# Performance work log

Measured on AMD Instinct MI355X. Metric: run time of the kernel, lower is better.

Reference implementation:

```python
import jax, jax.numpy as jnp
import numpy as np

B, C, H, W = 4, 128, 128, 128
K = 9          # 3x3 kernel taps
TAU, BETA = 0.5, 10.0


def conv3x3(x, w, b):
    # x: (B,Cin,H,W), w: (Cout,Cin,3,3), stride 1, padding 1
    y = jax.lax.conv_general_dilated(
        x, w, window_strides=(1, 1), padding=((1, 1), (1, 1)),
        dimension_numbers=('NCHW', 'OIHW', 'NCHW'))
    return y + b[None, :, None, None]


def bilinear_sample(x, py, px):
    # x: (B,C,H,W); py,px: (B,K,H,W) fractional coords -> (B,C,K,H,W), zero outside
    Hi, Wi = x.shape[2], x.shape[3]
    y0 = jnp.floor(py); x0 = jnp.floor(px)
    y1 = y0 + 1.0;      x1 = x0 + 1.0
    ly = py - y0; lx = px - x0
    hy = 1.0 - ly; hx = 1.0 - lx
    xf = x.reshape(x.shape[0], x.shape[1], -1)  # (B,C,HW)

    def corner(yc, xc, wgt):
        valid = (yc >= 0) & (yc <= Hi - 1) & (xc >= 0) & (xc <= Wi - 1)
        yi = jnp.clip(yc, 0, Hi - 1).astype(jnp.int32)
        xi = jnp.clip(xc, 0, Wi - 1).astype(jnp.int32)
        idx = (yi * Wi + xi).reshape(yc.shape[0], -1)  # (B, K*H*W)
        g = jax.vmap(lambda f, i: f[:, i])(xf, idx)    # (B,C,K*H*W)
        g = g.reshape(x.shape[0], x.shape[1], *yc.shape[1:])  # (B,C,K,H,W)
        return g * (wgt * valid.astype(wgt.dtype))[:, None]

    return (corner(y0, x0, hy * hx) + corner(y0, x1, hy * lx)
            + corner(y1, x0, ly * hx) + corner(y1, x1, ly * lx))


def modulated_dcn(x, offset, mask, w, b):
    # offset: (B,2K,H,W) layout (dy,dx) per tap; mask: (B,K,H,W)
    Bn, Cn, Hn, Wn = x.shape
    off = offset.reshape(Bn, K, 2, Hn, Wn)
    dy, dx = off[:, :, 0], off[:, :, 1]
    ky, kx = jnp.meshgrid(jnp.arange(3), jnp.arange(3), indexing='ij')
    base_y = (ky.reshape(-1) - 1).astype(x.dtype)  # dilation=1, padding=1, stride=1
    base_x = (kx.reshape(-1) - 1).astype(x.dtype)
    hh = jnp.arange(Hn, dtype=x.dtype)
    ww = jnp.arange(Wn, dtype=x.dtype)
    py = hh[None, None, :, None] + base_y[None, :, None, None] + dy  # (B,K,H,W)
    px = ww[None, None, None, :] + base_x[None, :, None, None] + dx
    samp = bilinear_sample(x, py, px) * mask[:, None]  # (B,C,K,H,W)
    out = jnp.einsum('bckhw,ock->bohw', samp, w.reshape(w.shape[0], w.shape[1], K))
    return out + b[None, :, None, None]


def setup_inputs() -> dict:
    key = jax.random.key(0)
    ks = jax.random.split(key, 8)
    x = jax.random.normal(ks[0], (B, C, H, W), dtype=jnp.float32)
    U = jax.random.uniform(ks[1], (B, 1, H, W), dtype=jnp.float32)
    # conv_offset_mask: (3*K, C+1, 3, 3); small scale -> offsets of O(1) pixel
    w_om = jax.random.normal(ks[2], (3 * K, C + 1, 3, 3), dtype=jnp.float32) * 0.01
    b_om = jnp.zeros((3 * K,), dtype=jnp.float32)
    kaiming = float(np.sqrt(2.0 / (C * 9)))
    w_dcn = jax.random.normal(ks[3], (C, C, 3, 3), dtype=jnp.float32) * kaiming
    b_dcn = jnp.zeros((C,), dtype=jnp.float32)
    w1 = jax.random.normal(ks[4], (C, C, 3, 3), dtype=jnp.float32) * kaiming
    b1 = jnp.zeros((C,), dtype=jnp.float32)
    w2 = jax.random.normal(ks[5], (C, C, 3, 3), dtype=jnp.float32) * float(np.sqrt(1.0 / (C * 9)))
    b2 = jnp.zeros((C,), dtype=jnp.float32)
    return {"x": x, "U": U, "w_om": w_om, "b_om": b_om, "w_dcn": w_dcn,
            "b_dcn": b_dcn, "w1": w1, "b1": b1, "w2": w2, "b2": b2}


def reference(x, U, w_om, b_om, w_dcn, b_dcn, w1, b1, w2, b2):
    U = jnp.clip(U, 0.0, 1.0)
    guide = jnp.concatenate([x, U], axis=1)                # (B,C+1,H,W)
    om = conv3x3(guide, w_om, b_om)                        # (B,3K,H,W)
    offset = om[:, :2 * K]
    mask = 2.0 * jax.nn.sigmoid(om[:, 2 * K:])
    z = modulated_dcn(x, offset, mask, w_dcn, b_dcn)
    r = jax.nn.relu(conv3x3(z, w1, b1))
    r = conv3x3(r, w2, b2)
    gate = jax.nn.sigmoid(BETA * (U - TAU))
    return jax.nn.relu(x + r * gate)
```

## Files before the change

### kernel.cpp

```cpp
#include <hip/hip_runtime.h>
#include <math.h>

typedef unsigned int uint;
typedef unsigned short ushort;
typedef __attribute__((ext_vector_type(8))) __bf16 bf16x8;
typedef __attribute__((ext_vector_type(2))) __bf16 bf16x2;
typedef __attribute__((ext_vector_type(4))) float f32x4;
typedef __attribute__((ext_vector_type(2))) float f32x2;

#define HW 16384

__device__ __forceinline__ ushort f2bf(float f) {
    uint u = __float_as_uint(f);
    u += 0x7fffu + ((u >> 16) & 1u);
    return (ushort)(u >> 16);
}
__device__ __forceinline__ void bhmap(int& b, int& h) {
    int lin = blockIdx.y * (int)gridDim.x + blockIdx.x;
    int n = (lin & 7) * 64 + (lin >> 3);
    h = n & 127;
    b = n >> 7;
}
__device__ __forceinline__ int swz(int row, int chunk) {
    return row * 128 + ((chunk ^ (row & 15)) << 3);
}
__device__ __forceinline__ void gl2lds16(const ushort* g, ushort* l) {
    __builtin_amdgcn_global_load_lds(
        (const __attribute__((address_space(1))) uint*)g,
        (__attribute__((address_space(3))) uint*)l,
        16, 0, 0);
}
__device__ __forceinline__ uint blend2(uint a, uint b, uint c, uint d,
                                       float w00, float w01, float w10, float w11) {
    f32x2 va = { __uint_as_float(a << 16), __uint_as_float(a & 0xffff0000u) };
    f32x2 vb = { __uint_as_float(b << 16), __uint_as_float(b & 0xffff0000u) };
    f32x2 vc = { __uint_as_float(c << 16), __uint_as_float(c & 0xffff0000u) };
    f32x2 vd = { __uint_as_float(d << 16), __uint_as_float(d & 0xffff0000u) };
    f32x2 v = va * w00 + vb * w01 + vc * w10 + vd * w11;
    bf16x2 pk; pk[0] = (__bf16)v[0]; pk[1] = (__bf16)v[1];
    uint r; __builtin_memcpy(&r, &pk, 4);
    return r;
}

__global__ __launch_bounds__(256) void prep_w(
    const float* __restrict__ wd, const float* __restrict__ w1,
    const float* __restrict__ w2, const float* __restrict__ wom,
    ushort* __restrict__ wdt, ushort* __restrict__ w1t,
    ushort* __restrict__ w2t, ushort* __restrict__ womt,
    float* __restrict__ womu)
{
    int i = blockIdx.x * 256 + threadIdx.x;
    if (i < 147456) {
        int k = i >> 14, oc = (i >> 7) & 127, d = i & 127;
        int ci = (((d >> 3) ^ (oc & 15)) << 3) | (d & 7);
        int s = (oc * 128 + ci) * 9 + k;
        wdt[i] = f2bf(wd[s]);
        w1t[i] = f2bf(w1[s]);
        w2t[i] = f2bf(w2[s]);
    }
    if (i < 36864) {
        int k = i >> 12, oc = (i >> 7) & 31, d = i & 127;
        int ci = (((d >> 3) ^ (oc & 15)) << 3) | (d & 7);
        womt[i] = (oc < 27) ? f2bf(wom[(oc * 129 + ci) * 9 + k]) : (ushort)0;
    }
    if (i < 288) {
        int k = i >> 5, oc = i & 31;
        womu[i] = (oc < 27) ? wom[(oc * 129 + 128) * 9 + k] : 0.f;
    }
}

__global__ __launch_bounds__(256) void prep_xt(
    const float* __restrict__ x, ushort* __restrict__ xt)
{
    int b, h; bhmap(b, h);
    const int tid = threadIdx.x;
    __shared__ __align__(16) ushort T[128 * 136];
    const int w0 = tid & 127, cg = tid >> 7;
#pragma unroll 4
    for (int it = 0; it < 64; it++) {
        int c = it * 2 + cg;
        float f = x[((size_t)(b * 128 + c)) * HW + h * 128 + w0];
        T[w0 * 136 + c] = f2bf(f);
    }
    __syncthreads();
    const int w1 = tid >> 1, half = tid & 1;
    uint4* dst = (uint4*)(xt + (((size_t)b * HW) + h * 128 + w1) * 128 + half * 64);
    const uint4* src = (const uint4*)&T[w1 * 136 + half * 64];
#pragma unroll
    for (int c8 = 0; c8 < 8; c8++) dst[c8] = src[c8];
}

__global__ __launch_bounds__(512, 4) void k_om(
    const ushort* __restrict__ xt, const float* __restrict__ U,
    const ushort* __restrict__ womt, const float* __restrict__ womu,
    const float* __restrict__ bom, float* __restrict__ omt)
{
    int b, h; bhmap(b, h);
    const int tid = threadIdx.x;
    const int wid = tid >> 6, lane = tid & 63, lq = lane & 15, quad = lane >> 4;
    const int pixbase = wid * 16;

    __shared__ __align__(16) ushort As[128 * 128];
    __shared__ __align__(16) ushort Bs[32 * 128];
    __shared__ float U3[3 * 130];
    __shared__ float wu[288];

    f32x4 acc[2];
#pragma unroll
    for (int j = 0; j < 2; j++)
#pragma unroll
        for (int r = 0; r < 4; r++) acc[j][r] = 0.f;

    for (int s = tid; s < 390; s += 512) {
        int r = s / 130, c = s % 130, gy = h - 1 + r, gx = c - 1;
        float v = 0.f;
        if ((unsigned)gy < 128u && (unsigned)gx < 128u) {
            v = U[(size_t)b * HW + gy * 128 + gx];
            v = fminf(fmaxf(v, 0.f), 1.f);
        }
        U3[s] = v;
    }
    if (tid < 288) wu[tid] = womu[tid];

    const int arow = tid >> 2, aq = tid & 3;
    for (int t9 = 0; t9 < 9; t9++) {
        int dy = t9 / 3 - 1, dx = t9 % 3 - 1;
        gl2lds16(womt + t9 * 4096 + tid * 8, &Bs[wid * 512]);
        int gy = h + dy, gx = arow + dx;
        if ((unsigned)gy < 128u && (unsigned)gx < 128u) {
            const uint4* src = (const uint4*)(xt + (((size_t)b * HW) + gy * 128 + gx) * 128 + aq * 32);
#pragma unroll
            for (int c = 0; c < 4; c++) *(uint4*)&As[swz(arow, aq * 4 + c)] = src[c];
        } else {
            uint4 zz = {0, 0, 0, 0};
#pragma unroll
            for (int c = 0; c < 4; c++) *(uint4*)&As[swz(arow, aq * 4 + c)] = zz;
        }
        __syncthreads();
#pragma unroll
        for (int kk = 0; kk < 4; kk++) {
            int chunk = kk * 4 + quad;
            bf16x8 av = *(const bf16x8*)&As[swz(pixbase + lq, chunk)];
            bf16x8 bv[2];
#pragma unroll
            for (int j = 0; j < 2; j++) bv[j] = *(const bf16x8*)&Bs[swz(j * 16 + lq, chunk)];
#pragma unroll
            for (int j = 0; j < 2; j++)
                acc[j] = __builtin_amdgcn_mfma_f32_16x16x32_bf16(av, bv[j], acc[j], 0, 0, 0);
        }
        __syncthreads();
    }

#pragma unroll
    for (int j = 0; j < 2; j++) {
        int oc = j * 16 + lq;
        if (oc < 27) {
            float bias = bom[oc];
#pragma unroll
            for (int r = 0; r < 4; r++) {
                int pix = pixbase + quad * 4 + r;
                float v = acc[j][r] + bias;
#pragma unroll
                for (int t = 0; t < 9; t++)
                    v += U3[(t / 3) * 130 + pix + (t % 3)] * wu[t * 32 + oc];
                if (oc >= 18) v = 2.f / (1.f + __expf(-v));
                omt[((size_t)b * HW + h * 128 + pix) * 32 + oc] = v;
            }
        }
    }
}

__global__ __launch_bounds__(512, 4) void k_dcn(
    const ushort* __restrict__ xt, const float* __restrict__ omt,
    const ushort* __restrict__ wdt, const float* __restrict__ bdcn,
    ushort* __restrict__ zt)
{
    int b, h; bhmap(b, h);
    const int tid = threadIdx.x;
    const int wid = tid >> 6, lane = tid & 63, lq = lane & 15, quad = lane >> 4;
    const int pixbase = (wid & 1) * 64, ocbase = (wid >> 1) * 32;

    __shared__ __align__(16) ushort As[128 * 128];
    __shared__ __align__(16) ushort Bs[128 * 128];
    __shared__ __align__(16) int tbl[2][128][8];

    const int sc = lane & 15;
    const int sp = lane >> 4;

    f32x4 acc[4][2];
#pragma unroll
    for (int i = 0; i < 4; i++)
#pragma unroll
        for (int j = 0; j < 2; j++)
#pragma unroll
            for (int r = 0; r < 4; r++) acc[i][j][r] = 0.f;

    const float* omrow = omt + ((size_t)b * HW + h * 128) * 32;
    const ushort* xtb = xt + (size_t)b * HW * 128;

    auto build = [&](int k, int buf) {
        if (tid < 128) {
            int p = tid;
            float dyv = omrow[p * 32 + 2 * k];
            float dxv = omrow[p * 32 + 2 * k + 1];
            float m   = omrow[p * 32 + 18 + k];
            float fy = (float)(h + k / 3 - 1) + dyv;
            float fx = (float)(p + k % 3 - 1) + dxv;
            float y0f = floorf(fy), x0f = floorf(fx);
            float ly = fy - y0f, lx = fx - x0f;
            float hy = 1.f - ly, hx = 1.f - lx;
            bool vy0 = (y0f >= 0.f) && (y0f <= 127.f);
            bool vy1 = (y0f >= -1.f) && (y0f <= 126.f);
            bool vx0 = (x0f >= 0.f) && (x0f <= 127.f);
            bool vx1 = (x0f >= -1.f) && (x0f <= 126.f);
            float w00 = (vy0 && vx0) ? hy * hx * m : 0.f;
            float w01 = (vy0 && vx1) ? hy * lx * m : 0.f;
            float w10 = (vy1 && vx0) ? ly * hx * m : 0.f;
            float w11 = (vy1 && vx1) ? ly * lx * m : 0.f;
            int iy0 = min(max((int)y0f, 0), 127);
            int iy1 = min(max((int)y0f + 1, 0), 127);
            int ix0 = min(max((int)x0f, 0), 127);
            int ix1 = min(max((int)x0f + 1, 0), 127);
            int* tp = &tbl[buf][p][0];
            tp[0] = (iy0 * 128 + ix0) * 128;
            tp[1] = (iy0 * 128 + ix1) * 128;
            tp[2] = (iy1 * 128 + ix0) * 128;
            tp[3] = (iy1 * 128 + ix1) * 128;
            ((float*)tp)[4] = w00; ((float*)tp)[5] = w01;
            ((float*)tp)[6] = w10; ((float*)tp)[7] = w11;
        }
    };

    build(0, 0);
    __syncthreads();

    for (int k = 0; k < 9; k++) {
        const int buf = k & 1;
        const ushort* basep = xtb + sc * 8;

        uint4 g[4][4];
        f32x4 wvr[4];
#pragma unroll
        for (int r = 0; r < 4; r++) {
            int p = r * 32 + wid * 4 + sp;
            int4 off = *(const int4*)&tbl[buf][p][0];
            wvr[r] = *(const f32x4*)((const float*)&tbl[buf][p][0] + 4);
            g[r][0] = *(const uint4*)(basep + off.x);
            g[r][1] = *(const uint4*)(basep + off.y);
            g[r][2] = *(const uint4*)(basep + off.z);
            g[r][3] = *(const uint4*)(basep + off.w);
        }
        {
            const ushort* wsrc = wdt + (size_t)k * 16384;
#pragma unroll
            for (int c = 0; c < 4; c++)
                gl2lds16(wsrc + c * 4096 + tid * 8, &Bs[c * 4096 + wid * 512]);
        }
#pragma unroll
        for (int r = 0; r < 4; r++) {
            int p = r * 32 + wid * 4 + sp;
            uint4 st;
            st.x = blend2(g[r][0].x, g[r][1].x, g[r][2].x, g[r][3].x,
                          wvr[r][0], wvr[r][1], wvr[r][2], wvr[r][3]);
            st.y = blend2(g[r][0].y, g[r][1].y, g[r][2].y, g[r][3].y,
                          wvr[r][0], wvr[r][1], wvr[r][2], wvr[r][3]);
            st.z = blend2(g[r][0].z, g[r][1].z, g[r][2].z, g[r][3].z,
                          wvr[r][0], wvr[r][1], wvr[r][2], wvr[r][3]);
            st.w = blend2(g[r][0].w, g[r][1].w, g[r][2].w, g[r][3].w,
                          wvr[r][0], wvr[r][1], wvr[r][2], wvr[r][3]);
            *(uint4*)&As[swz(p, sc)] = st;
        }
        __syncthreads();
        if (k < 8) build(k + 1, buf ^ 1);
#pragma unroll
        for (int kk = 0; kk < 4; kk++) {
            int chunk = kk * 4 + quad;
            bf16x8 av[4], bv[2];
#pragma unroll
            for (int i = 0; i < 4; i++) av[i] = *(const bf16x8*)&As[swz(pixbase + i * 16 + lq, chunk)];
#pragma unroll
            for (int j = 0; j < 2; j++) bv[j] = *(const bf16x8*)&Bs[swz(ocbase + j * 16 + lq, chunk)];
#pragma unroll
            for (int i = 0; i < 4; i++)
#pragma unroll
                for (int j = 0; j < 2; j++)
                    acc[i][j] = __builtin_amdgcn_mfma_f32_16x16x32_bf16(av[i], bv[j], acc[i][j], 0, 0, 0);
        }
        __syncthreads();
    }

    size_t prow = ((size_t)b * HW + h * 128) * 128;
#pragma unroll
    for (int j = 0; j < 2; j++) {
        int oc = ocbase + j * 16 + lq;
        float bias = bdcn[oc];
#pragma unroll
        for (int i = 0; i < 4; i++)
#pragma unroll
            for (int r = 0; r < 4; r++) {
                int pix = pixbase + i * 16 + quad * 4 + r;
                zt[prow + (size_t)pix * 128 + oc] = f2bf(acc[i][j][r] + bias);
            }
    }
}

__global__ __launch_bounds__(512, 4) void k_conv1(
    const ushort* __restrict__ zt, const ushort* __restrict__ w1t,
    const float* __restrict__ b1, ushort* __restrict__ r1t)
{
    int b, h; bhmap(b, h);
    const int tid = threadIdx.x;
    const int wid = tid >> 6, lane = tid & 63, lq = lane & 15, quad = lane >> 4;
    const int pixbase = (wid & 1) * 64, ocbase = (wid >> 1) * 32;

    __shared__ __align__(16) ushort As[128 * 128];
    __shared__ __align__(16) ushort Bs[128 * 128];

    f32x4 acc[4][2];
#pragma unroll
    for (int i = 0; i < 4; i++)
#pragma unroll
        for (int j = 0; j < 2; j++)
#pragma unroll
            for (int r = 0; r < 4; r++) acc[i][j][r] = 0.f;

    const int row = tid >> 2, q = tid & 3;
    for (int t9 = 0; t9 < 9; t9++) {
        int dy = t9 / 3 - 1, dx = t9 % 3 - 1;
        {
            const ushort* wsrc = w1t + (size_t)t9 * 16384;
#pragma unroll
            for (int c = 0; c < 4; c++)
                gl2lds16(wsrc + c * 4096 + tid * 8, &Bs[c * 4096 + wid * 512]);
        }
        int gy = h + dy, gx = row + dx;
        if ((unsigned)gy < 128u && (unsigned)gx < 128u) {
            const uint4* src = (const uint4*)(zt + (((size_t)b * HW) + gy * 128 + gx) * 128 + q * 32);
#pragma unroll
            for (int c = 0; c < 4; c++) *(uint4*)&As[swz(row, q * 4 + c)] = src[c];
        } else {
            uint4 zz = {0, 0, 0, 0};
#pragma unroll
            for (int c = 0; c < 4; c++) *(uint4*)&As[swz(row, q * 4 + c)] = zz;
        }
        __syncthreads();
#pragma unroll
        for (int kk = 0; kk < 4; kk++) {
            int chunk = kk * 4 + quad;
            bf16x8 av[4], bv[2];
#pragma unroll
            for (int i = 0; i < 4; i++) av[i] = *(const bf16x8*)&As[swz(pixbase + i * 16 + lq, chunk)];
#pragma unroll
            for (int j = 0; j < 2; j++) bv[j] = *(const bf16x8*)&Bs[swz(ocbase + j * 16 + lq, chunk)];
#pragma unroll
            for (int i = 0; i < 4; i++)
#pragma unroll
                for (int j = 0; j < 2; j++)
                    acc[i][j] = __builtin_amdgcn_mfma_f32_16x16x32_bf16(av[i], bv[j], acc[i][j], 0, 0, 0);
        }
        __syncthreads();
    }

    size_t prow = ((size_t)b * HW + h * 128) * 128;
#pragma unroll
    for (int j = 0; j < 2; j++) {
        int oc = ocbase + j * 16 + lq;
        float bias = b1[oc];
#pragma unroll
        for (int i = 0; i < 4; i++)
#pragma unroll
            for (int r = 0; r < 4; r++) {
                int pix = pixbase + i * 16 + quad * 4 + r;
                r1t[prow + (size_t)pix * 128 + oc] = f2bf(fmaxf(acc[i][j][r] + bias, 0.f));
            }
    }
}

__global__ __launch_bounds__(512, 4) void k_conv2(
    const ushort* __restrict__ r1t, const ushort* __restrict__ w2t,
    const float* __restrict__ b2, const float* __restrict__ x,
    const float* __restrict__ U, float* __restrict__ out)
{
    int b, h; bhmap(b, h);
    const int tid = threadIdx.x;
    const int wid = tid >> 6, lane = tid & 63, lq = lane & 15, quad = lane >> 4;
    const int mbase = (wid & 1) * 64;
    const int nbase = (wid >> 1) * 32;

    __shared__ __align__(16) ushort As[128 * 128];
    __shared__ __align__(16) ushort Bs[128 * 128];

    f32x4 acc[4][2];
#pragma unroll
    for (int i = 0; i < 4; i++)
#pragma unroll
        for (int j = 0; j < 2; j++)
#pragma unroll
            for (int r = 0; r < 4; r++) acc[i][j][r] = 0.f;

    const int row = tid >> 2, q = tid & 3;
    for (int t9 = 0; t9 < 9; t9++) {
        int dy = t9 / 3 - 1, dx = t9 % 3 - 1;
        {
            const ushort* wsrc = w2t + (size_t)t9 * 16384;
#pragma unroll
            for (int c = 0; c < 4; c++)
                gl2lds16(wsrc + c * 4096 + tid * 8, &As[c * 4096 + wid * 512]);
        }
        int gy = h + dy, gx = row + dx;
        if ((unsigned)gy < 128u && (unsigned)gx < 128u) {
            const uint4* src = (const uint4*)(r1t + (((size_t)b * HW) + gy * 128 + gx) * 128 + q * 32);
#pragma unroll
            for (int c = 0; c < 4; c++) *(uint4*)&Bs[swz(row, q * 4 + c)] = src[c];
        } else {
            uint4 zz = {0, 0, 0, 0};
#pragma unroll
            for (int c = 0; c < 4; c++) *(uint4*)&Bs[swz(row, q * 4 + c)] = zz;
        }
        __syncthreads();
#pragma unroll
        for (int kk = 0; kk < 4; kk++) {
            int chunk = kk * 4 + quad;
            bf16x8 av[4], bv[2];
#pragma unroll
            for (int i = 0; i < 4; i++) av[i] = *(const bf16x8*)&As[swz(mbase + i * 16 + lq, chunk)];
#pragma unroll
            for (int j = 0; j < 2; j++) bv[j] = *(const bf16x8*)&Bs[swz(nbase + j * 16 + lq, chunk)];
#pragma unroll
            for (int i = 0; i < 4; i++)
#pragma unroll
                for (int j = 0; j < 2; j++)
                    acc[i][j] = __builtin_amdgcn_mfma_f32_16x16x32_bf16(av[i], bv[j], acc[i][j], 0, 0, 0);
        }
        __syncthreads();
    }

#pragma unroll
    for (int j = 0; j < 2; j++) {
        int pix = nbase + j * 16 + lq;
        float u = U[(size_t)b * HW + h * 128 + pix];
        u = fminf(fmaxf(u, 0.f), 1.f);
        float g = 1.f / (1.f + __expf(-10.f * (u - 0.5f)));
#pragma unroll
        for (int i = 0; i < 4; i++) {
            f32x4 b4 = *(const f32x4*)&b2[mbase + i * 16 + quad * 4];
#pragma unroll
            for (int r = 0; r < 4; r++) {
                int oc = mbase + i * 16 + quad * 4 + r;
                size_t idx = ((size_t)(b * 128 + oc)) * HW + h * 128 + pix;
                float v = acc[i][j][r] + b4[r];
                out[idx] = fmaxf(x[idx] + v * g, 0.f);
            }
        }
    }
}

extern "C" void kernel_launch(void* const* d_in, const int* in_sizes, int n_in,
                              void* d_out, int out_size, void* d_ws, size_t ws_size,
                              hipStream_t stream)
{
    const float* x     = (const float*)d_in[0];
    const float* U     = (const float*)d_in[1];
    const float* w_om  = (const float*)d_in[2];
    const float* b_om  = (const float*)d_in[3];
    const float* w_dcn = (const float*)d_in[4];
    const float* b_dcn = (const float*)d_in[5];
    const float* w1    = (const float*)d_in[6];
    const float* b1    = (const float*)d_in[7];
    const float* w2    = (const float*)d_in[8];
    const float* b2    = (const float*)d_in[9];
    float* out = (float*)d_out;

    char* p = (char*)d_ws;
    ushort* xt   = (ushort*)p; p += (size_t)4 * HW * 128 * 2;
    ushort* zt   = (ushort*)p; p += (size_t)4 * HW * 128 * 2;
    ushort* r1t  = (ushort*)p; p += (size_t)4 * HW * 128 * 2;
    float*  omt  = (float*)p;  p += (size_t)4 * HW * 32 * 4;
    ushort* wdt  = (ushort*)p; p += 147456 * 2;
    ushort* w1t  = (ushort*)p; p += 147456 * 2;
    ushort* w2t  = (ushort*)p; p += 147456 * 2;
    ushort* womt = (ushort*)p; p += 36864 * 2;
    float*  womu = (float*)p;  p += 288 * 4;

    prep_w<<<576, 256, 0, stream>>>(w_dcn, w1, w2, w_om, wdt, w1t, w2t, womt, womu);
    prep_xt<<<dim3(128, 4), 256, 0, stream>>>(x, xt);
    k_om<<<dim3(128, 4), 512, 0, stream>>>(xt, U, womt, womu, b_om, omt);
    k_dcn<<<dim3(128, 4), 512, 0, stream>>>(xt, omt, wdt, b_dcn, zt);
    k_conv1<<<dim3(128, 4), 512, 0, stream>>>(zt, w1t, b1, r1t);
    k_conv2<<<dim3(128, 4), 512, 0, stream>>>(r1t, w2t, b2, x, U, out);
}
```

Baseline: 262.2 us.

## Double-buffer DCN sampled tile and weights to overlap gathers with MFMA

```diff
diff --git a/kernel.cpp b/kernel.cpp
--- a/kernel.cpp
+++ b/kernel.cpp
@@ -41,6 +41,16 @@
     uint r; __builtin_memcpy(&r, &pk, 4);
     return r;
 }
+__device__ __forceinline__ uint4 blend8(const uint4 q0, const uint4 q1,
+                                        const uint4 q2, const uint4 q3,
+                                        const f32x4 wv) {
+    uint4 st;
+    st.x = blend2(q0.x, q1.x, q2.x, q3.x, wv[0], wv[1], wv[2], wv[3]);
+    st.y = blend2(q0.y, q1.y, q2.y, q3.y, wv[0], wv[1], wv[2], wv[3]);
+    st.z = blend2(q0.z, q1.z, q2.z, q3.z, wv[0], wv[1], wv[2], wv[3]);
+    st.w = blend2(q0.w, q1.w, q2.w, q3.w, wv[0], wv[1], wv[2], wv[3]);
+    return st;
+}
 
 __global__ __launch_bounds__(256) void prep_w(
     const float* __restrict__ wd, const float* __restrict__ w1,
@@ -170,7 +180,7 @@
     }
 }
 
-__global__ __launch_bounds__(512, 4) void k_dcn(
+__global__ __launch_bounds__(512, 2) void k_dcn(
     const ushort* __restrict__ xt, const float* __restrict__ omt,
     const ushort* __restrict__ wdt, const float* __restrict__ bdcn,
     ushort* __restrict__ zt)
@@ -180,8 +190,8 @@
     const int wid = tid >> 6, lane = tid & 63, lq = lane & 15, quad = lane >> 4;
     const int pixbase = (wid & 1) * 64, ocbase = (wid >> 1) * 32;
 
-    __shared__ __align__(16) ushort As[128 * 128];
-    __shared__ __align__(16) ushort Bs[128 * 128];
+    __shared__ __align__(16) ushort As[2][128 * 128];
+    __shared__ __align__(16) ushort Bs[2][128 * 128];
     __shared__ __align__(16) int tbl[2][128][8];
 
     const int sc = lane & 15;
@@ -197,6 +207,7 @@
 
     const float* omrow = omt + ((size_t)b * HW + h * 128) * 32;
     const ushort* xtb = xt + (size_t)b * HW * 128;
+    const ushort* basep = xtb + sc * 8;
 
     auto build = [&](int k, int buf) {
         if (tid < 128) {
@@ -233,59 +244,76 @@
 
     build(0, 0);
     __syncthreads();
-
-    for (int k = 0; k < 9; k++) {
-        const int buf = k & 1;
-        const ushort* basep = xtb + sc * 8;
-
-        uint4 g[4][4];
-        f32x4 wvr[4];
+    {
+        const ushort* wsrc = wdt;
+#pragma unroll
+        for (int c = 0; c < 4; c++)
+            gl2lds16(wsrc + c * 4096 + tid * 8, &Bs[0][c * 4096 + wid * 512]);
+        uint4 g[4][4]; f32x4 wvr[4];
 #pragma unroll
         for (int r = 0; r < 4; r++) {
             int p = r * 32 + wid * 4 + sp;
-            int4 off = *(const int4*)&tbl[buf][p][0];
-            wvr[r] = *(const f32x4*)((const float*)&tbl[buf][p][0] + 4);
+            int4 off = *(const int4*)&tbl[0][p][0];
+            wvr[r] = *(const f32x4*)((const float*)&tbl[0][p][0] + 4);
             g[r][0] = *(const uint4*)(basep + off.x);
             g[r][1] = *(const uint4*)(basep + off.y);
             g[r][2] = *(const uint4*)(basep + off.z);
             g[r][3] = *(const uint4*)(basep + off.w);
         }
-        {
-            const ushort* wsrc = wdt + (size_t)k * 16384;
-#pragma unroll
-            for (int c = 0; c < 4; c++)
-                gl2lds16(wsrc + c * 4096 + tid * 8, &Bs[c * 4096 + wid * 512]);
-        }
 #pragma unroll
         for (int r = 0; r < 4; r++) {
             int p = r * 32 + wid * 4 + sp;
-            uint4 st;
-            st.x = blend2(g[r][0].x, g[r][1].x, g[r][2].x, g[r][3].x,
-                          wvr[r][0], wvr[r][1], wvr[r][2], wvr[r][3]);
-            st.y = blend2(g[r][0].y, g[r][1].y, g[r][2].y, g[r][3].y,
-                          wvr[r][0], wvr[r][1], wvr[r][2], wvr[r][3]);
-            st.z = blend2(g[r][0].z, g[r][1].z, g[r][2].z, g[r][3].z,
-                          wvr[r][0], wvr[r][1], wvr[r][2], wvr[r][3]);
-            st.w = blend2(g[r][0].w, g[r][1].w, g[r][2].w, g[r][3].w,
-                          wvr[r][0], wvr[r][1], wvr[r][2], wvr[r][3]);
-            *(uint4*)&As[swz(p, sc)] = st;
-        }
-        __syncthreads();
-        if (k < 8) build(k + 1, buf ^ 1);
+            *(uint4*)&As[0][swz(p, sc)] = blend8(g[r][0], g[r][1], g[r][2], g[r][3], wvr[r]);
+        }
+        build(1, 1);
+    }
+    __syncthreads();
+
+    for (int k = 0; k < 9; k++) {
+        const int cur = k & 1, nxt = cur ^ 1;
+        const bool pf = (k < 8);
+
+        if (pf) {
+            const ushort* wsrc = wdt + (size_t)(k + 1) * 16384;
+#pragma unroll
+            for (int c = 0; c < 4; c++)
+                gl2lds16(wsrc + c * 4096 + tid * 8, &Bs[nxt][c * 4096 + wid * 512]);
+        }
+        uint4 g[4][4]; f32x4 wvr[4];
+        if (pf) {
+#pragma unroll
+            for (int r = 0; r < 4; r++) {
+                int p = r * 32 + wid * 4 + sp;
+                int4 off = *(const int4*)&tbl[nxt][p][0];
+                wvr[r] = *(const f32x4*)((const float*)&tbl[nxt][p][0] + 4);
+                g[r][0] = *(const uint4*)(basep + off.x);
+                g[r][1] = *(const uint4*)(basep + off.y);
+                g[r][2] = *(const uint4*)(basep + off.z);
+                g[r][3] = *(const uint4*)(basep + off.w);
+            }
+        }
 #pragma unroll
         for (int kk = 0; kk < 4; kk++) {
             int chunk = kk * 4 + quad;
             bf16x8 av[4], bv[2];
 #pragma unroll
-            for (int i = 0; i < 4; i++) av[i] = *(const bf16x8*)&As[swz(pixbase + i * 16 + lq, chunk)];
-#pragma unroll
-            for (int j = 0; j < 2; j++) bv[j] = *(const bf16x8*)&Bs[swz(ocbase + j * 16 + lq, chunk)];
+            for (int i = 0; i < 4; i++) av[i] = *(const bf16x8*)&As[cur][swz(pixbase + i * 16 + lq, chunk)];
+#pragma unroll
+            for (int j = 0; j < 2; j++) bv[j] = *(const bf16x8*)&Bs[cur][swz(ocbase + j * 16 + lq, chunk)];
 #pragma unroll
             for (int i = 0; i < 4; i++)
 #pragma unroll
                 for (int j = 0; j < 2; j++)
                     acc[i][j] = __builtin_amdgcn_mfma_f32_16x16x32_bf16(av[i], bv[j], acc[i][j], 0, 0, 0);
         }
+        if (pf) {
+#pragma unroll
+            for (int r = 0; r < 4; r++) {
+                int p = r * 32 + wid * 4 + sp;
+                *(uint4*)&As[nxt][swz(p, sc)] = blend8(g[r][0], g[r][1], g[r][2], g[r][3], wvr[r]);
+            }
+        }
+        if (k < 7) build(k + 2, cur);
         __syncthreads();
     }
 
```

New measurement: 225.6 us. -14.0%, faster.
